# Kernel optimization log

Measured on AMD Instinct MI355X. Metric: run time of the kernel, lower is better.

## Reference

```python
import jax, jax.numpy as jnp
import numpy as np
import math

INPUT_SIZE = 1024
OUTPUT_SIZE = 1024
QK_SIZE = 1024
B, S = 4, 2048


def setup_inputs() -> dict:
    key = jax.random.key(0)
    ks = jax.random.split(key, 7)
    scale = 1.0 / math.sqrt(INPUT_SIZE)
    return {
        "x": jax.random.normal(ks[0], (B, S, INPUT_SIZE), dtype=jnp.float32),
        "Wq": jax.random.uniform(ks[1], (QK_SIZE, INPUT_SIZE), minval=-scale, maxval=scale, dtype=jnp.float32),
        "bq": jax.random.uniform(ks[2], (QK_SIZE,), minval=-scale, maxval=scale, dtype=jnp.float32),
        "Wk": jax.random.uniform(ks[3], (QK_SIZE, INPUT_SIZE), minval=-scale, maxval=scale, dtype=jnp.float32),
        "bk": jax.random.uniform(ks[4], (QK_SIZE,), minval=-scale, maxval=scale, dtype=jnp.float32),
        "Wv": jax.random.uniform(ks[5], (OUTPUT_SIZE, INPUT_SIZE), minval=-scale, maxval=scale, dtype=jnp.float32),
        "bv": jax.random.uniform(ks[6], (OUTPUT_SIZE,), minval=-scale, maxval=scale, dtype=jnp.float32),
    }


def reference(x, Wq, bq, Wk, bk, Wv, bv):
    # torch Linear: y = x @ W.T + b
    q = jnp.einsum('bsd,ed->bse', x, Wq) + bq  # [B,S,QK]
    k = jnp.einsum('bsd,ed->bse', x, Wk) + bk  # [B,S,QK]
    v = jnp.einsum('bsd,ed->bse', x, Wv) + bv  # [B,S,OUT]
    inv_sqrt_d = 1.0 / math.sqrt(QK_SIZE)
    scores = jnp.einsum('bqe,bke->bqk', q, k) * inv_sqrt_d  # [B,S,S]
    attn = jax.nn.softmax(scores, axis=-1)
    return jnp.einsum('bqk,bko->bqo', attn, v)  # [B,S,OUT]
```

## Files before the change

kernel.cpp:

```cpp
#include <hip/hip_runtime.h>
#include <stdint.h>

typedef unsigned short u16;
typedef __attribute__((ext_vector_type(8))) __bf16 bf16x8;
typedef __attribute__((ext_vector_type(4))) float f32x4;

__device__ __forceinline__ u16 f2bf(float f) {
    union { float f; uint32_t u; } v; v.f = f;
    uint32_t r = (v.u + 0x7FFFu + ((v.u >> 16) & 1u)) >> 16;
    return (u16)r;
}

__device__ __forceinline__ void lds_fence() {
    __asm__ volatile("s_waitcnt lgkmcnt(0)" ::: "memory");
}

#define BAR()  __asm__ volatile("s_barrier" ::: "memory")
#define VMW(N) __asm__ volatile("s_waitcnt vmcnt(" #N ")" ::: "memory")

template<int MODE>
__global__ __launch_bounds__(512, 2) void gemm8(
    const u16* __restrict__ A, const u16* __restrict__ Bt,
    const float* __restrict__ b0, const float* __restrict__ b1, const float* __restrict__ b2,
    u16* __restrict__ o0, u16* __restrict__ o1, u16* __restrict__ o2,
    float* __restrict__ o3, float* __restrict__ lsum,
    int M, int N, int K, long sA, long sB, long sC, float scale)
{
    extern __shared__ __align__(16) u16 smem[];
    constexpr int NJ = (MODE == 3) ? 2 : 4;

    const int t = threadIdx.x;
    const int lane = t & 63;
    const int wave = t >> 6;
    const int wm = wave >> 2;
    const int wn = wave & 3;

    const int id = blockIdx.x;
    const int xcd = id & 7;
    const int s = id >> 3;
    int bm, bn;
    long bz;
    if (MODE == 0) {
        bm = (xcd * 4 + (s & 3)) * 256;
        bn = (s >> 2) * 256;
        bz = 0;
    } else if (MODE == 2) {
        bz = xcd >> 1;
        bm = ((xcd & 1) * 4 + (s & 3)) * 256;
        bn = (s >> 2) * 256;
    } else {
        bz = xcd >> 1;
        bm = ((xcd & 1) * 4 + (s & 3)) * 256;
        bn = (s >> 2) * 128;
    }

    const u16* Ab = A + bz * sA;
    const u16* Bb = Bt + bz * sB;

    f32x4 acc[8][NJ];
#pragma unroll
    for (int i = 0; i < 8; ++i)
#pragma unroll
        for (int j = 0; j < NJ; ++j)
            acc[i][j] = (f32x4){0.f, 0.f, 0.f, 0.f};

    const int trow = t >> 2;
    const int gcol = ((t & 3) * 8) ^ ((trow & 8) << 1);
    const u16* aRow = Ab + (long)(bm + trow) * K + gcol;
    const u16* bRow = Bb + (long)(bn + trow) * K + gcol;

    auto stage1 = [&](int buf, int kt, int isB, int h, int kb) {
        const u16* g = (isB ? bRow : aRow) + (long)(h * 128) * K + kt * 64 + kb * 32;
        u16* d = smem + buf * 32768 + isB * 16384 + h * 8192 + kb * 4096 + t * 8;
        __builtin_amdgcn_global_load_lds(
            (const __attribute__((address_space(1))) void*)g,
            (__attribute__((address_space(3))) void*)d, 16, 0, 0);
    };

    const int fm = lane & 15;
    const int fcol = ((lane >> 4) * 8) ^ ((fm & 8) << 1);
    const int aB = wm * 8192 + fm * 32 + fcol;
    const int bB = (MODE == 3)
        ? 16384 + wn * 1024 + fm * 32 + fcol
        : 16384 + (wn >> 1) * 8192 + (wn & 1) * 2048 + fm * 32 + fcol;

    bf16x8 aCur[4], aNxt[4], bCur[NJ], bNxt[NJ];

#define RD_A(DST, BUF, MH, KH) do { \
    _Pragma("unroll") for (int mi = 0; mi < 4; ++mi) \
        DST[mi] = *(const bf16x8*)&smem[(BUF)*32768 + aB + (KH)*4096 + (MH)*2048 + mi*512]; \
} while (0)

#define RD_B(DST, BUF, KH) do { \
    _Pragma("unroll") for (int ni = 0; ni < NJ; ++ni) \
        DST[ni] = *(const bf16x8*)&smem[(BUF)*32768 + bB + (KH)*4096 + ni*512]; \
} while (0)

#define PH(MH, FA, FB) do { \
    __builtin_amdgcn_s_setprio(1); \
    _Pragma("unroll") for (int mi = 0; mi < 4; ++mi) \
    _Pragma("unroll") for (int ni = 0; ni < NJ; ++ni) \
        acc[(MH)*4+mi][ni] = __builtin_amdgcn_mfma_f32_16x16x32_bf16( \
            FA[mi], FB[ni], acc[(MH)*4+mi][ni], 0, 0, 0); \
    __builtin_amdgcn_s_setprio(0); \
} while (0)

    const int NT = K >> 6;
    const int NI = NT >> 1;

    stage1(0, 0, 1, 0, 0); if (MODE != 3) stage1(0, 0, 1, 1, 0);
    stage1(0, 0, 0, 0, 0); stage1(0, 0, 0, 1, 0);
    stage1(0, 0, 1, 0, 1); if (MODE != 3) stage1(0, 0, 1, 1, 1);
    stage1(0, 0, 0, 0, 1); stage1(0, 0, 0, 1, 1);
    stage1(1, 1, 1, 0, 0); if (MODE != 3) stage1(1, 1, 1, 1, 0);
    stage1(1, 1, 0, 0, 0); stage1(1, 1, 0, 1, 0);
    if (MODE == 3) { VMW(6); } else { VMW(8); }
    BAR();
    RD_A(aCur, 0, 0, 0); RD_B(bCur, 0, 0);

    for (int i = 0; i < NI; ++i) {
        const int t1 = 2 * i + 1;
        int t2 = 2 * i + 2; if (t2 >= NT) t2 -= NT;
        int t3 = 2 * i + 3; if (t3 >= NT) t3 -= NT;

        PH(0, aCur, bCur);
        RD_A(aNxt, 0, 1, 0);
        stage1(1, t1, 1, 0, 1); if (MODE != 3) stage1(1, t1, 1, 1, 1);
        if (MODE == 3) { VMW(4); } else { VMW(6); }
        BAR();
        PH(1, aNxt, bCur);
        RD_A(aCur, 0, 0, 1); RD_B(bNxt, 0, 1);
        stage1(1, t1, 0, 0, 1); stage1(1, t1, 0, 1, 1);
        BAR();
        PH(0, aCur, bNxt);
        RD_A(aNxt, 0, 1, 1);
        stage1(0, t2, 1, 0, 0); if (MODE != 3) stage1(0, t2, 1, 1, 0);
        if (MODE == 3) { VMW(4); } else { VMW(6); }
        BAR();
        PH(1, aNxt, bNxt);
        RD_A(aCur, 1, 0, 0); RD_B(bCur, 1, 0);
        stage1(0, t2, 0, 0, 0); stage1(0, t2, 0, 1, 0);
        BAR();
        PH(0, aCur, bCur);
        RD_A(aNxt, 1, 1, 0);
        stage1(0, t2, 1, 0, 1); if (MODE != 3) stage1(0, t2, 1, 1, 1);
        if (MODE == 3) { VMW(4); } else { VMW(6); }
        BAR();
        PH(1, aNxt, bCur);
        RD_A(aCur, 1, 0, 1); RD_B(bNxt, 1, 1);
        stage1(0, t2, 0, 0, 1); stage1(0, t2, 0, 1, 1);
        BAR();
        PH(0, aCur, bNxt);
        RD_A(aNxt, 1, 1, 1);
        stage1(1, t3, 1, 0, 0); if (MODE != 3) stage1(1, t3, 1, 1, 0);
        if (MODE == 3) { VMW(4); } else { VMW(6); }
        BAR();
        PH(1, aNxt, bNxt);
        RD_A(aCur, 0, 0, 0); RD_B(bCur, 0, 0);
        stage1(1, t3, 0, 0, 0); stage1(1, t3, 0, 1, 0);
        BAR();
    }

    VMW(0);
    BAR();

    const int cm = (lane >> 4) * 4;
    const int cn = lane & 15;
    u16* Ew = smem + wave * 8192;
    const int gmb = bm + wm * 128;

    if constexpr (MODE == 3) {
        float* Fw = (float*)Ew;
        const int cnb3 = bn + wn * 32;
#pragma unroll
        for (int p = 0; p < 4; ++p) {
            if (p) lds_fence();
#pragma unroll
            for (int m2 = 0; m2 < 2; ++m2) {
                const int mi = p * 2 + m2;
#pragma unroll
                for (int ni = 0; ni < 2; ++ni)
#pragma unroll
                    for (int r = 0; r < 4; ++r)
                        Fw[(m2 * 16 + cm + r) * 36 + ni * 16 + cn] = acc[mi][ni][r];
            }
#pragma unroll
            for (int it = 0; it < 4; ++it) {
                const int row = it * 8 + (lane >> 3);
                const int c4 = (lane & 7) * 4;
                f32x4 w = *(const f32x4*)&Fw[row * 36 + c4];
                const int gm = gmb + p * 32 + row;
                const float inv = __builtin_amdgcn_rcpf(lsum[bz * 2048 + gm]);
                w[0] *= inv; w[1] *= inv; w[2] *= inv; w[3] *= inv;
                *(f32x4*)&o3[bz * sC + (long)gm * N + cnb3 + c4] = w;
            }
        }
    } else if (MODE == 0 && (bn >> 10) == 2) {
        const int ebase = (bn & 1023) + wn * 64;
        float bb[4];
#pragma unroll
        for (int ni = 0; ni < 4; ++ni) bb[ni] = b2[ebase + ni * 16 + cn];
        const long bgi = gmb >> 11;
        const int sbase = gmb & 2047;
#pragma unroll
        for (int p = 0; p < 2; ++p) {
            if (p) lds_fence();
#pragma unroll
            for (int m4 = 0; m4 < 4; ++m4) {
                const int mi = p * 4 + m4;
#pragma unroll
                for (int ni = 0; ni < 4; ++ni) {
                    ushort4 pk;
                    pk.x = f2bf(acc[mi][ni][0] + bb[ni]);
                    pk.y = f2bf(acc[mi][ni][1] + bb[ni]);
                    pk.z = f2bf(acc[mi][ni][2] + bb[ni]);
                    pk.w = f2bf(acc[mi][ni][3] + bb[ni]);
                    *(ushort4*)&Ew[(ni * 16 + cn) * 72 + m4 * 16 + cm] = pk;
                }
            }
#pragma unroll
            for (int it = 0; it < 8; ++it) {
                const int e = it * 8 + (lane >> 3);
                const int s8 = (lane & 7) * 8;
                const uint4 w = *(const uint4*)&Ew[e * 72 + s8];
                *(uint4*)&o2[(((bgi << 10) + ebase + e) << 11) + sbase + p * 64 + s8] = w;
            }
        }
    } else if (MODE == 0) {
        const int sec = bn >> 10;
        u16* C = sec ? o1 : o0;
        const float* bias = sec ? b1 : b0;
        const int ncol0 = (bn & 1023) + wn * 64;
        float bb[4];
#pragma unroll
        for (int ni = 0; ni < 4; ++ni) bb[ni] = bias[ncol0 + ni * 16 + cn];
#pragma unroll
        for (int p = 0; p < 2; ++p) {
            if (p) lds_fence();
#pragma unroll
            for (int m4 = 0; m4 < 4; ++m4) {
                const int mi = p * 4 + m4;
#pragma unroll
                for (int ni = 0; ni < 4; ++ni)
#pragma unroll
                    for (int r = 0; r < 4; ++r)
                        Ew[(m4 * 16 + cm + r) * 72 + ni * 16 + cn] = f2bf(acc[mi][ni][r] + bb[ni]);
            }
#pragma unroll
            for (int it = 0; it < 8; ++it) {
                const int row = it * 8 + (lane >> 3);
                const int c8 = (lane & 7) * 8;
                const uint4 w = *(const uint4*)&Ew[row * 72 + c8];
                *(uint4*)&C[(long)(gmb + p * 64 + row) * 1024 + ncol0 + c8] = w;
            }
        }
    } else {
        const int cnb = bn + wn * 64;
#pragma unroll
        for (int mi = 0; mi < 8; ++mi)
#pragma unroll
            for (int ni = 0; ni < 4; ++ni)
#pragma unroll
                for (int r = 0; r < 4; ++r)
                    acc[mi][ni][r] = __expf(acc[mi][ni][r] * scale);
#pragma unroll
        for (int mi = 0; mi < 8; ++mi) {
#pragma unroll
            for (int r = 0; r < 4; ++r) {
                float sm = acc[mi][0][r] + acc[mi][1][r] + acc[mi][2][r] + acc[mi][3][r];
                sm += __shfl_xor(sm, 1);
                sm += __shfl_xor(sm, 2);
                sm += __shfl_xor(sm, 4);
                sm += __shfl_xor(sm, 8);
                if (cn == 0)
                    atomicAdd(&lsum[bz * 2048 + gmb + mi * 16 + cm + r], sm);
            }
        }
#pragma unroll
        for (int p = 0; p < 2; ++p) {
            if (p) lds_fence();
#pragma unroll
            for (int m4 = 0; m4 < 4; ++m4) {
                const int mi = p * 4 + m4;
#pragma unroll
                for (int ni = 0; ni < 4; ++ni)
#pragma unroll
                    for (int r = 0; r < 4; ++r)
                        Ew[(m4 * 16 + cm + r) * 72 + ni * 16 + cn] = f2bf(acc[mi][ni][r]);
            }
#pragma unroll
            for (int it = 0; it < 8; ++it) {
                const int row = it * 8 + (lane >> 3);
                const int c8 = (lane & 7) * 8;
                const uint4 w = *(const uint4*)&Ew[row * 72 + c8];
                *(uint4*)&o0[bz * sC + (long)(gmb + p * 64 + row) * N + cnb + c8] = w;
            }
        }
    }
}

#undef RD_A
#undef RD_B
#undef PH

__global__ __launch_bounds__(256) void cvt_all(
    const float* __restrict__ x, const float* __restrict__ wq,
    const float* __restrict__ wk, const float* __restrict__ wv,
    u16* __restrict__ xb, u16* __restrict__ wb, float* __restrict__ lsum)
{
    const int b = blockIdx.x;
    if (b >= 11264) {
        const long i = (long)(b - 11264) * 1024 + threadIdx.x * 4;
        *(f32x4*)(lsum + i) = (f32x4){0.f, 0.f, 0.f, 0.f};
        return;
    }
    const float* src; u16* dst; long base;
    if (b < 8192)       { src = x;  dst = xb;             base = (long)b * 1024; }
    else if (b < 9216)  { src = wq; dst = wb;             base = (long)(b - 8192) * 1024; }
    else if (b < 10240) { src = wk; dst = wb + (1 << 20); base = (long)(b - 9216) * 1024; }
    else                { src = wv; dst = wb + (2 << 20); base = (long)(b - 10240) * 1024; }
    const long i = base + threadIdx.x * 4;
    const f32x4 f = *(const f32x4*)(src + i);
    ushort4 o;
    o.x = f2bf(f[0]); o.y = f2bf(f[1]); o.z = f2bf(f[2]); o.w = f2bf(f[3]);
    *(ushort4*)(dst + i) = o;
}

extern "C" void kernel_launch(void* const* d_in, const int* in_sizes, int n_in,
                              void* d_out, int out_size, void* d_ws, size_t ws_size,
                              hipStream_t stream) {
    const float* x  = (const float*)d_in[0];
    const float* Wq = (const float*)d_in[1];
    const float* bq = (const float*)d_in[2];
    const float* Wk = (const float*)d_in[3];
    const float* bk = (const float*)d_in[4];
    const float* Wv = (const float*)d_in[5];
    const float* bv = (const float*)d_in[6];
    float* out = (float*)d_out;

    const int B = 4, S = 2048, D = 1024, E = 1024;
    const int M = B * S;
    const size_t LDS = 131072;

    u16* xb  = (u16*)d_ws;
    u16* wb  = xb  + (size_t)M * D;
    u16* qb  = wb  + (size_t)3 * E * D;
    u16* kb  = qb  + (size_t)M * E;
    u16* vbT = kb  + (size_t)M * E;
    u16* sb  = vbT + (size_t)M * E;
    float* lsum = (float*)(sb + (size_t)M * S);

    static bool attr_done = false;
    if (!attr_done) {
        (void)hipFuncSetAttribute((const void*)gemm8<0>, hipFuncAttributeMaxDynamicSharedMemorySize, (int)LDS);
        (void)hipFuncSetAttribute((const void*)gemm8<2>, hipFuncAttributeMaxDynamicSharedMemorySize, (int)LDS);
        (void)hipFuncSetAttribute((const void*)gemm8<3>, hipFuncAttributeMaxDynamicSharedMemorySize, (int)LDS);
        attr_done = true;
    }

    cvt_all<<<11272, 256, 0, stream>>>(x, Wq, Wk, Wv, xb, wb, lsum);

    dim3 blk(512);
    gemm8<0><<<384, blk, LDS, stream>>>(
        xb, wb, bq, bk, bv, qb, kb, vbT, nullptr, nullptr, M, 3 * E, D, 0, 0, 0, 1.f);
    gemm8<2><<<256, blk, LDS, stream>>>(
        qb, kb, nullptr, nullptr, nullptr, sb, nullptr, nullptr, nullptr, lsum,
        S, S, E, (long)S * E, (long)S * E, (long)S * S, 0.03125f);
    gemm8<3><<<256, blk, LDS, stream>>>(
        sb, vbT, nullptr, nullptr, nullptr, nullptr, nullptr, nullptr, out, lsum,
        S, E, S, (long)S * S, (long)E * S, (long)S * E, 1.f);
}
```

Measured before the change: 227.9 us.

## Load B fragments directly from global into registers and shrink tile to 128x256

The GEMM kernel now stages only the A tile through LDS and fetches B operand fragments straight from global memory into registers with inline global_load_dwordx4, double-buffered across even and odd K steps. The block tile changes to 128x256 with a 4x4 MFMA accumulator per wave, so the first two GEMMs launch twice as many blocks. The epilogues are simplified to match. This is meant to cut LDS traffic and barrier work, but it depends on uncoalesced global reads for B hitting in cache and gives less reuse per block.

New measurement: 356.5 us. 1.56x slower.

```diff
diff --git a/kernel.cpp b/kernel.cpp
--- a/kernel.cpp
+++ b/kernel.cpp
@@ -15,8 +15,9 @@
     __asm__ volatile("s_waitcnt lgkmcnt(0)" ::: "memory");
 }
 
-#define BAR()  __asm__ volatile("s_barrier" ::: "memory")
-#define VMW(N) __asm__ volatile("s_waitcnt vmcnt(" #N ")" ::: "memory")
+#define BAR()   __asm__ volatile("s_barrier" ::: "memory")
+#define VMW(N)  __asm__ volatile("s_waitcnt vmcnt(" #N ")" ::: "memory")
+#define SCHB()  __builtin_amdgcn_sched_barrier(0)
 
 template<int MODE>
 __global__ __launch_bounds__(512, 2) void gemm8(
@@ -27,7 +28,6 @@
     int M, int N, int K, long sA, long sB, long sC, float scale)
 {
     extern __shared__ __align__(16) u16 smem[];
-    constexpr int NJ = (MODE == 3) ? 2 : 4;
 
     const int t = threadIdx.x;
     const int lane = t & 63;
@@ -41,124 +41,98 @@
     int bm, bn;
     long bz;
     if (MODE == 0) {
-        bm = (xcd * 4 + (s & 3)) * 256;
-        bn = (s >> 2) * 256;
+        bm = xcd * 8 + (s & 7);
+        bn = s >> 3;
         bz = 0;
     } else if (MODE == 2) {
         bz = xcd >> 1;
-        bm = ((xcd & 1) * 4 + (s & 3)) * 256;
-        bn = (s >> 2) * 256;
+        bm = (xcd & 1) * 8 + (s & 7);
+        bn = s >> 3;
     } else {
         bz = xcd >> 1;
-        bm = ((xcd & 1) * 4 + (s & 3)) * 256;
-        bn = (s >> 2) * 128;
-    }
+        bm = (xcd & 1) * 8 + (s & 7);
+        bn = s >> 3;
+    }
+    const int row0 = bm * 128;
+    const int col0 = bn * 256;
 
     const u16* Ab = A + bz * sA;
     const u16* Bb = Bt + bz * sB;
 
-    f32x4 acc[8][NJ];
-#pragma unroll
-    for (int i = 0; i < 8; ++i)
-#pragma unroll
-        for (int j = 0; j < NJ; ++j)
+    f32x4 acc[4][4];
+#pragma unroll
+    for (int i = 0; i < 4; ++i)
+#pragma unroll
+        for (int j = 0; j < 4; ++j)
             acc[i][j] = (f32x4){0.f, 0.f, 0.f, 0.f};
 
     const int trow = t >> 2;
     const int gcol = ((t & 3) * 8) ^ ((trow & 8) << 1);
-    const u16* aRow = Ab + (long)(bm + trow) * K + gcol;
-    const u16* bRow = Bb + (long)(bn + trow) * K + gcol;
-
-    auto stage1 = [&](int buf, int kt, int isB, int h, int kb) {
-        const u16* g = (isB ? bRow : aRow) + (long)(h * 128) * K + kt * 64 + kb * 32;
-        u16* d = smem + buf * 32768 + isB * 16384 + h * 8192 + kb * 4096 + t * 8;
+    const u16* aRow = Ab + (long)(row0 + trow) * K + gcol;
+
+    auto stageA = [&](int buf, int kt, int kb) {
+        const u16* g = aRow + kt * 64 + kb * 32;
+        u16* d = smem + buf * 8192 + kb * 4096 + t * 8;
         __builtin_amdgcn_global_load_lds(
             (const __attribute__((address_space(1))) void*)g,
             (__attribute__((address_space(3))) void*)d, 16, 0, 0);
     };
 
     const int fm = lane & 15;
-    const int fcol = ((lane >> 4) * 8) ^ ((fm & 8) << 1);
-    const int aB = wm * 8192 + fm * 32 + fcol;
-    const int bB = (MODE == 3)
-        ? 16384 + wn * 1024 + fm * 32 + fcol
-        : 16384 + (wn >> 1) * 8192 + (wn & 1) * 2048 + fm * 32 + fcol;
-
-    bf16x8 aCur[4], aNxt[4], bCur[NJ], bNxt[NJ];
-
-#define RD_A(DST, BUF, MH, KH) do { \
+    const int fk = (lane >> 4) * 8;
+    const int fcol = fk ^ ((fm & 8) << 1);
+    const int aB = (wm * 64 + fm) * 32 + fcol;
+
+    const u16* bp[4];
+#pragma unroll
+    for (int ni = 0; ni < 4; ++ni)
+        bp[ni] = Bb + (long)(col0 + wn * 64 + ni * 16 + fm) * K + fk;
+
+    f32x4 fbE[4][2], fbO[4][2];
+
+#define GATHER(FB) do { \
+    _Pragma("unroll") for (int ni = 0; ni < 4; ++ni) { \
+        asm volatile("global_load_dwordx4 %0, %2, off\n\t" \
+                     "global_load_dwordx4 %1, %2, off offset:64" \
+            : "=&v"(FB[ni][0]), "=&v"(FB[ni][1]) : "v"(bp[ni]) : "memory"); \
+    } \
+    _Pragma("unroll") for (int ni = 0; ni < 4; ++ni) bp[ni] += 64; \
+} while (0)
+
+#define PHASE(BUF, FB, T2) do { \
+    SCHB(); \
+    bf16x8 fa[4][2]; \
     _Pragma("unroll") for (int mi = 0; mi < 4; ++mi) \
-        DST[mi] = *(const bf16x8*)&smem[(BUF)*32768 + aB + (KH)*4096 + (MH)*2048 + mi*512]; \
-} while (0)
-
-#define RD_B(DST, BUF, KH) do { \
-    _Pragma("unroll") for (int ni = 0; ni < NJ; ++ni) \
-        DST[ni] = *(const bf16x8*)&smem[(BUF)*32768 + bB + (KH)*4096 + ni*512]; \
-} while (0)
-
-#define PH(MH, FA, FB) do { \
+    _Pragma("unroll") for (int kh = 0; kh < 2; ++kh) \
+        fa[mi][kh] = *(const bf16x8*)&smem[(BUF) * 8192 + kh * 4096 + aB + mi * 512]; \
     __builtin_amdgcn_s_setprio(1); \
     _Pragma("unroll") for (int mi = 0; mi < 4; ++mi) \
-    _Pragma("unroll") for (int ni = 0; ni < NJ; ++ni) \
-        acc[(MH)*4+mi][ni] = __builtin_amdgcn_mfma_f32_16x16x32_bf16( \
-            FA[mi], FB[ni], acc[(MH)*4+mi][ni], 0, 0, 0); \
+    _Pragma("unroll") for (int ni = 0; ni < 4; ++ni) \
+    _Pragma("unroll") for (int kh = 0; kh < 2; ++kh) \
+        acc[mi][ni] = __builtin_amdgcn_mfma_f32_16x16x32_bf16( \
+            fa[mi][kh], __builtin_bit_cast(bf16x8, FB[ni][kh]), acc[mi][ni], 0, 0, 0); \
     __builtin_amdgcn_s_setprio(0); \
+    GATHER(FB); \
+    stageA(BUF, (T2), 0); stageA(BUF, (T2), 1); \
+    VMW(10); \
+    BAR(); \
 } while (0)
 
     const int NT = K >> 6;
     const int NI = NT >> 1;
 
-    stage1(0, 0, 1, 0, 0); if (MODE != 3) stage1(0, 0, 1, 1, 0);
-    stage1(0, 0, 0, 0, 0); stage1(0, 0, 0, 1, 0);
-    stage1(0, 0, 1, 0, 1); if (MODE != 3) stage1(0, 0, 1, 1, 1);
-    stage1(0, 0, 0, 0, 1); stage1(0, 0, 0, 1, 1);
-    stage1(1, 1, 1, 0, 0); if (MODE != 3) stage1(1, 1, 1, 1, 0);
-    stage1(1, 1, 0, 0, 0); stage1(1, 1, 0, 1, 0);
-    if (MODE == 3) { VMW(6); } else { VMW(8); }
+    GATHER(fbE);
+    stageA(0, 0, 0); stageA(0, 0, 1);
+    GATHER(fbO);
+    stageA(1, 1, 0); stageA(1, 1, 1);
+    VMW(10);
     BAR();
-    RD_A(aCur, 0, 0, 0); RD_B(bCur, 0, 0);
 
     for (int i = 0; i < NI; ++i) {
-        const int t1 = 2 * i + 1;
         int t2 = 2 * i + 2; if (t2 >= NT) t2 -= NT;
         int t3 = 2 * i + 3; if (t3 >= NT) t3 -= NT;
-
-        PH(0, aCur, bCur);
-        RD_A(aNxt, 0, 1, 0);
-        stage1(1, t1, 1, 0, 1); if (MODE != 3) stage1(1, t1, 1, 1, 1);
-        if (MODE == 3) { VMW(4); } else { VMW(6); }
-        BAR();
-        PH(1, aNxt, bCur);
-        RD_A(aCur, 0, 0, 1); RD_B(bNxt, 0, 1);
-        stage1(1, t1, 0, 0, 1); stage1(1, t1, 0, 1, 1);
-        BAR();
-        PH(0, aCur, bNxt);
-        RD_A(aNxt, 0, 1, 1);
-        stage1(0, t2, 1, 0, 0); if (MODE != 3) stage1(0, t2, 1, 1, 0);
-        if (MODE == 3) { VMW(4); } else { VMW(6); }
-        BAR();
-        PH(1, aNxt, bNxt);
-        RD_A(aCur, 1, 0, 0); RD_B(bCur, 1, 0);
-        stage1(0, t2, 0, 0, 0); stage1(0, t2, 0, 1, 0);
-        BAR();
-        PH(0, aCur, bCur);
-        RD_A(aNxt, 1, 1, 0);
-        stage1(0, t2, 1, 0, 1); if (MODE != 3) stage1(0, t2, 1, 1, 1);
-        if (MODE == 3) { VMW(4); } else { VMW(6); }
-        BAR();
-        PH(1, aNxt, bCur);
-        RD_A(aCur, 1, 0, 1); RD_B(bNxt, 1, 1);
-        stage1(0, t2, 0, 0, 1); stage1(0, t2, 0, 1, 1);
-        BAR();
-        PH(0, aCur, bNxt);
-        RD_A(aNxt, 1, 1, 1);
-        stage1(1, t3, 1, 0, 0); if (MODE != 3) stage1(1, t3, 1, 1, 0);
-        if (MODE == 3) { VMW(4); } else { VMW(6); }
-        BAR();
-        PH(1, aNxt, bNxt);
-        RD_A(aCur, 0, 0, 0); RD_B(bCur, 0, 0);
-        stage1(1, t3, 0, 0, 0); stage1(1, t3, 0, 1, 0);
-        BAR();
+        PHASE(0, fbE, t2);
+        PHASE(1, fbO, t3);
     }
 
     VMW(0);
@@ -167,104 +141,91 @@
     const int cm = (lane >> 4) * 4;
     const int cn = lane & 15;
     u16* Ew = smem + wave * 8192;
-    const int gmb = bm + wm * 128;
+    const int row0w = row0 + wm * 64;
+    const int col0w = col0 + wn * 64;
 
     if constexpr (MODE == 3) {
         float* Fw = (float*)Ew;
-        const int cnb3 = bn + wn * 32;
-#pragma unroll
-        for (int p = 0; p < 4; ++p) {
+#pragma unroll
+        for (int p = 0; p < 2; ++p) {
             if (p) lds_fence();
 #pragma unroll
             for (int m2 = 0; m2 < 2; ++m2) {
                 const int mi = p * 2 + m2;
 #pragma unroll
-                for (int ni = 0; ni < 2; ++ni)
+                for (int ni = 0; ni < 4; ++ni)
 #pragma unroll
                     for (int r = 0; r < 4; ++r)
-                        Fw[(m2 * 16 + cm + r) * 36 + ni * 16 + cn] = acc[mi][ni][r];
+                        Fw[(m2 * 16 + cm + r) * 68 + ni * 16 + cn] = acc[mi][ni][r];
             }
 #pragma unroll
-            for (int it = 0; it < 4; ++it) {
-                const int row = it * 8 + (lane >> 3);
-                const int c4 = (lane & 7) * 4;
-                f32x4 w = *(const f32x4*)&Fw[row * 36 + c4];
-                const int gm = gmb + p * 32 + row;
+            for (int it = 0; it < 8; ++it) {
+                const int row = it * 4 + (lane >> 4);
+                const int c4 = (lane & 15) * 4;
+                f32x4 w = *(const f32x4*)&Fw[row * 68 + c4];
+                const int gm = row0w + p * 32 + row;
                 const float inv = __builtin_amdgcn_rcpf(lsum[bz * 2048 + gm]);
                 w[0] *= inv; w[1] *= inv; w[2] *= inv; w[3] *= inv;
-                *(f32x4*)&o3[bz * sC + (long)gm * N + cnb3 + c4] = w;
+                *(f32x4*)&o3[bz * sC + (long)gm * N + col0w + c4] = w;
             }
         }
-    } else if (MODE == 0 && (bn >> 10) == 2) {
-        const int ebase = (bn & 1023) + wn * 64;
+    } else if (MODE == 0 && (bn >> 2) == 2) {
+        const int ebase = (bn & 3) * 256 + wn * 64;
         float bb[4];
 #pragma unroll
         for (int ni = 0; ni < 4; ++ni) bb[ni] = b2[ebase + ni * 16 + cn];
-        const long bgi = gmb >> 11;
-        const int sbase = gmb & 2047;
-#pragma unroll
-        for (int p = 0; p < 2; ++p) {
-            if (p) lds_fence();
-#pragma unroll
-            for (int m4 = 0; m4 < 4; ++m4) {
-                const int mi = p * 4 + m4;
-#pragma unroll
-                for (int ni = 0; ni < 4; ++ni) {
-                    ushort4 pk;
-                    pk.x = f2bf(acc[mi][ni][0] + bb[ni]);
-                    pk.y = f2bf(acc[mi][ni][1] + bb[ni]);
-                    pk.z = f2bf(acc[mi][ni][2] + bb[ni]);
-                    pk.w = f2bf(acc[mi][ni][3] + bb[ni]);
-                    *(ushort4*)&Ew[(ni * 16 + cn) * 72 + m4 * 16 + cm] = pk;
-                }
+        const long bgi = row0w >> 11;
+        const int sbase = row0w & 2047;
+#pragma unroll
+        for (int mi = 0; mi < 4; ++mi)
+#pragma unroll
+            for (int ni = 0; ni < 4; ++ni) {
+                ushort4 pk;
+                pk.x = f2bf(acc[mi][ni][0] + bb[ni]);
+                pk.y = f2bf(acc[mi][ni][1] + bb[ni]);
+                pk.z = f2bf(acc[mi][ni][2] + bb[ni]);
+                pk.w = f2bf(acc[mi][ni][3] + bb[ni]);
+                *(ushort4*)&Ew[(ni * 16 + cn) * 72 + mi * 16 + cm] = pk;
             }
 #pragma unroll
-            for (int it = 0; it < 8; ++it) {
-                const int e = it * 8 + (lane >> 3);
-                const int s8 = (lane & 7) * 8;
-                const uint4 w = *(const uint4*)&Ew[e * 72 + s8];
-                *(uint4*)&o2[(((bgi << 10) + ebase + e) << 11) + sbase + p * 64 + s8] = w;
-            }
+        for (int it = 0; it < 8; ++it) {
+            const int e = it * 8 + (lane >> 3);
+            const int s8 = (lane & 7) * 8;
+            const uint4 w = *(const uint4*)&Ew[e * 72 + s8];
+            *(uint4*)&o2[(((bgi << 10) + ebase + e) << 11) + sbase + s8] = w;
         }
     } else if (MODE == 0) {
-        const int sec = bn >> 10;
+        const int sec = bn >> 2;
         u16* C = sec ? o1 : o0;
         const float* bias = sec ? b1 : b0;
-        const int ncol0 = (bn & 1023) + wn * 64;
+        const int ncol0 = (bn & 3) * 256 + wn * 64;
         float bb[4];
 #pragma unroll
         for (int ni = 0; ni < 4; ++ni) bb[ni] = bias[ncol0 + ni * 16 + cn];
 #pragma unroll
-        for (int p = 0; p < 2; ++p) {
-            if (p) lds_fence();
-#pragma unroll
-            for (int m4 = 0; m4 < 4; ++m4) {
-                const int mi = p * 4 + m4;
-#pragma unroll
-                for (int ni = 0; ni < 4; ++ni)
-#pragma unroll
-                    for (int r = 0; r < 4; ++r)
-                        Ew[(m4 * 16 + cm + r) * 72 + ni * 16 + cn] = f2bf(acc[mi][ni][r] + bb[ni]);
-            }
-#pragma unroll
-            for (int it = 0; it < 8; ++it) {
-                const int row = it * 8 + (lane >> 3);
-                const int c8 = (lane & 7) * 8;
-                const uint4 w = *(const uint4*)&Ew[row * 72 + c8];
-                *(uint4*)&C[(long)(gmb + p * 64 + row) * 1024 + ncol0 + c8] = w;
-            }
+        for (int mi = 0; mi < 4; ++mi)
+#pragma unroll
+            for (int ni = 0; ni < 4; ++ni)
+#pragma unroll
+                for (int r = 0; r < 4; ++r)
+                    Ew[(mi * 16 + cm + r) * 72 + ni * 16 + cn] = f2bf(acc[mi][ni][r] + bb[ni]);
+#pragma unroll
+        for (int it = 0; it < 8; ++it) {
+            const int row = it * 8 + (lane >> 3);
+            const int c8 = (lane & 7) * 8;
+            const uint4 w = *(const uint4*)&Ew[row * 72 + c8];
+            *(uint4*)&C[(long)(row0w + row) * 1024 + ncol0 + c8] = w;
         }
     } else {
-        const int cnb = bn + wn * 64;
-#pragma unroll
-        for (int mi = 0; mi < 8; ++mi)
+#pragma unroll
+        for (int mi = 0; mi < 4; ++mi)
 #pragma unroll
             for (int ni = 0; ni < 4; ++ni)
 #pragma unroll
                 for (int r = 0; r < 4; ++r)
                     acc[mi][ni][r] = __expf(acc[mi][ni][r] * scale);
 #pragma unroll
-        for (int mi = 0; mi < 8; ++mi) {
+        for (int mi = 0; mi < 4; ++mi) {
 #pragma unroll
             for (int r = 0; r < 4; ++r) {
                 float sm = acc[mi][0][r] + acc[mi][1][r] + acc[mi][2][r] + acc[mi][3][r];
@@ -273,35 +234,28 @@
                 sm += __shfl_xor(sm, 4);
                 sm += __shfl_xor(sm, 8);
                 if (cn == 0)
-                    atomicAdd(&lsum[bz * 2048 + gmb + mi * 16 + cm + r], sm);
+                    atomicAdd(&lsum[bz * 2048 + row0w + mi * 16 + cm + r], sm);
             }
         }
 #pragma unroll
-        for (int p = 0; p < 2; ++p) {
-            if (p) lds_fence();
-#pragma unroll
-            for (int m4 = 0; m4 < 4; ++m4) {
-                const int mi = p * 4 + m4;
-#pragma unroll
-                for (int ni = 0; ni < 4; ++ni)
-#pragma unroll
-                    for (int r = 0; r < 4; ++r)
-                        Ew[(m4 * 16 + cm + r) * 72 + ni * 16 + cn] = f2bf(acc[mi][ni][r]);
-            }
-#pragma unroll
-            for (int it = 0; it < 8; ++it) {
-                const int row = it * 8 + (lane >> 3);
-                const int c8 = (lane & 7) * 8;
-                const uint4 w = *(const uint4*)&Ew[row * 72 + c8];
-                *(uint4*)&o0[bz * sC + (long)(gmb + p * 64 + row) * N + cnb + c8] = w;
-            }
-        }
-    }
-}
-
-#undef RD_A
-#undef RD_B
-#undef PH
+        for (int mi = 0; mi < 4; ++mi)
+#pragma unroll
+            for (int ni = 0; ni < 4; ++ni)
+#pragma unroll
+                for (int r = 0; r < 4; ++r)
+                    Ew[(mi * 16 + cm + r) * 72 + ni * 16 + cn] = f2bf(acc[mi][ni][r]);
+#pragma unroll
+        for (int it = 0; it < 8; ++it) {
+            const int row = it * 8 + (lane >> 3);
+            const int c8 = (lane & 7) * 8;
+            const uint4 w = *(const uint4*)&Ew[row * 72 + c8];
+            *(uint4*)&o0[bz * sC + (long)(row0w + row) * N + col0w + c8] = w;
+        }
+    }
+}
+
+#undef GATHER
+#undef PHASE
 
 __global__ __launch_bounds__(256) void cvt_all(
     const float* __restrict__ x, const float* __restrict__ wq,
@@ -361,9 +315,9 @@
     cvt_all<<<11272, 256, 0, stream>>>(x, Wq, Wk, Wv, xb, wb, lsum);
 
     dim3 blk(512);
-    gemm8<0><<<384, blk, LDS, stream>>>(
+    gemm8<0><<<768, blk, LDS, stream>>>(
         xb, wb, bq, bk, bv, qb, kb, vbT, nullptr, nullptr, M, 3 * E, D, 0, 0, 0, 1.f);
-    gemm8<2><<<256, blk, LDS, stream>>>(
+    gemm8<2><<<512, blk, LDS, stream>>>(
         qb, kb, nullptr, nullptr, nullptr, sb, nullptr, nullptr, nullptr, lsum,
         S, S, E, (long)S * E, (long)S * E, (long)S * S, 0.03125f);
     gemm8<3><<<256, blk, LDS, stream>>>(
```
